# Kernel optimization log

Hardware: AMD Instinct MI355X
Metric: run time of the kernel (lower is better)

Reference implementation:

```python
import jax, jax.numpy as jnp
import numpy as np

B, CIN, COUT, K, SDIM, H, W = 8, 512, 256, 3, 512, 64, 64


def _blur_kernel():
    k = jnp.array([1.0, 3.0, 3.0, 1.0], dtype=jnp.float32)
    k = k[None, :] * k[:, None]
    k = k / k.sum()
    return k * 4.0  # upsample_factor ** 2


def setup_inputs() -> dict:
    key = jax.random.key(0)
    ks = jax.random.split(key, 4)
    return {
        "x": jax.random.normal(ks[0], (B, CIN, H, W), jnp.float32),
        "style": jax.random.normal(ks[1], (B, SDIM), jnp.float32),
        "weight": jax.random.normal(ks[2], (1, COUT, CIN, K, K), jnp.float32),
        "mod_weight": jax.random.normal(ks[3], (CIN, SDIM), jnp.float32),
        "mod_bias": jnp.ones((CIN,), jnp.float32),
    }


def reference(x, style, weight, mod_weight, mod_bias):
    b, cin, h, w = x.shape
    cout = weight.shape[1]
    k = weight.shape[-1]
    scale = 1.0 / np.sqrt(cin * k * k)          # fan_in of conv weight
    mod_scale = 1.0 / np.sqrt(mod_weight.shape[1])  # EqualLinear scale

    # modulation: EqualLinear(style) -> [B, Cin]
    s = style @ (mod_weight * mod_scale).T + mod_bias

    # per-sample modulated + demodulated weight [B, Cout, Cin, K, K]
    wmod = scale * weight * s[:, None, :, None, None]
    demod = jax.lax.rsqrt(jnp.sum(wmod * wmod, axis=(2, 3, 4)) + 1e-8)
    wmod = wmod * demod[:, :, None, None, None]

    # conv_transpose2d(stride=2, padding=0) == dilated conv with lhs_dilation=2,
    # padding K-1 on each side, spatially flipped kernel. Output (H-1)*2 + K.
    wflip = jnp.flip(wmod, axis=(-2, -1))

    def per_sample(xi, wi):
        return jax.lax.conv_general_dilated(
            xi[None], wi, window_strides=(1, 1),
            padding=[(k - 1, k - 1)] * 2, lhs_dilation=(2, 2),
            dimension_numbers=("NCHW", "OIHW", "NCHW"))[0]

    out = jax.vmap(per_sample)(x, wflip)  # [B, Cout, 2H+1, 2W+1] for K=3

    # Blur (upfirdn2d, up=1): torch does conv2d with flip(kernel);
    # lax conv is also correlation, so use flipped kernel, depthwise.
    bk = jnp.flip(_blur_kernel(), (0, 1))
    p = 4 - 2 - (k - 1)
    pad0 = (p + 1) // 2 + 1
    pad1 = p // 2 + 1
    wblur = jnp.broadcast_to(bk[None, None], (cout, 1, 4, 4))
    out = jax.lax.conv_general_dilated(
        out, wblur, (1, 1), [(pad0, pad1), (pad0, pad1)],
        feature_group_count=cout,
        dimension_numbers=("NCHW", "OIHW", "NCHW"))
    return out  # [B, Cout, 2H, 2W]
```

## Files before the change

### kernel.cpp

```cpp
#include <hip/hip_runtime.h>
#include <hip/hip_bf16.h>
#include <stdint.h>

typedef unsigned short u16;
typedef __attribute__((ext_vector_type(8))) short short8;
typedef __attribute__((ext_vector_type(4))) float floatx4;

__device__ __forceinline__ u16 f2bf(float f) {
    union { unsigned int i; float f; } v; v.f = f;
    unsigned int r = v.i + 0x7fff + ((v.i >> 16) & 1);
    return (u16)(r >> 16);
}

#define OFF_S    0
#define OFF_DEM  16384
#define OFF_W2   32768
#define OFF_BM   1048576
#define OFF_XMT  16777216

__global__ void k_style(const float* __restrict__ style, const float* __restrict__ mw,
                        const float* __restrict__ mb, float* __restrict__ S) {
    int g = blockIdx.x * 4 + (threadIdx.x >> 6);
    int lane = threadIdx.x & 63;
    int b = g >> 9, ci = g & 511;
    const float* sr = style + b * 512 + lane * 8;
    const float* wr = mw + ci * 512 + lane * 8;
    float4 s0 = *(const float4*)(sr);
    float4 s1 = *(const float4*)(sr + 4);
    float4 w0 = *(const float4*)(wr);
    float4 w1 = *(const float4*)(wr + 4);
    float acc = s0.x * w0.x + s0.y * w0.y + s0.z * w0.z + s0.w * w0.w
              + s1.x * w1.x + s1.y * w1.y + s1.z * w1.z + s1.w * w1.w;
    #pragma unroll
    for (int o = 32; o; o >>= 1) acc += __shfl_xor(acc, o, 64);
    if (lane == 0) S[g] = acc * 0.044194173824159216f + mb[ci];
}

__global__ void k_w2(const float* __restrict__ w, float* __restrict__ W2) {
    int t = blockIdx.x * 256 + threadIdx.x;
    const float* p = w + t * 9;
    float a = 0.f;
    #pragma unroll
    for (int i = 0; i < 9; ++i) { float v = p[i]; a += v * v; }
    W2[t] = a;
}

__global__ void k_demod(const float* __restrict__ W2, const float* __restrict__ S,
                        float* __restrict__ D) {
    int g = blockIdx.x * 4 + (threadIdx.x >> 6);
    int lane = threadIdx.x & 63;
    int b = g >> 8, co = g & 255;
    const float* wr = W2 + co * 512 + lane * 8;
    const float* sr = S + b * 512 + lane * 8;
    float4 w0 = *(const float4*)(wr);
    float4 w1 = *(const float4*)(wr + 4);
    float4 s0 = *(const float4*)(sr);
    float4 s1 = *(const float4*)(sr + 4);
    float a = w0.x * s0.x * s0.x + w0.y * s0.y * s0.y + w0.z * s0.z * s0.z + w0.w * s0.w * s0.w
            + w1.x * s1.x * s1.x + w1.y * s1.y * s1.y + w1.z * s1.z * s1.z + w1.w * s1.w * s1.w;
    #pragma unroll
    for (int o = 32; o; o >>= 1) a += __shfl_xor(a, o, 64);
    if (lane == 0) D[g] = 0.014731391274719738f * rsqrtf(a * (1.0f / 4608.0f) + 1e-8f);
}

__global__ void k_bmat(const float* __restrict__ Wt, u16* __restrict__ Bm) {
    __shared__ float wl[2304];
    int blk = blockIdx.x;
    int tid = threadIdx.x;
    int ci0 = (blk & 1) * 256;
    int co  = (blk >> 1) & 255;
    int p   = blk >> 9;
    int py = p >> 1, px = p & 1;
    int wbase = co * 4608 + ci0 * 9;
    #pragma unroll
    for (int j = 0; j < 9; ++j) wl[j * 256 + tid] = Wt[wbase + j * 256 + tid];
    __syncthreads();
    const float KT[2][3][3] = {
        {{0.f,1.f,3.f},{3.f,3.f,1.f},{1.f,0.f,0.f}},
        {{0.f,0.f,1.f},{1.f,3.f,3.f},{3.f,1.f,0.f}}
    };
    float wv[3][3];
    #pragma unroll
    for (int a = 0; a < 3; ++a)
        #pragma unroll
        for (int bq = 0; bq < 3; ++bq) wv[a][bq] = wl[tid * 9 + a * 3 + bq];
    int ci = ci0 + tid;
    int n = py * 512 + co * 2 + px;
    size_t base = (size_t)n * 4608 + ci;
    #pragma unroll
    for (int dyi = 0; dyi < 3; ++dyi) {
        #pragma unroll
        for (int dxi = 0; dxi < 3; ++dxi) {
            float val = 0.f;
            #pragma unroll
            for (int a = 0; a < 3; ++a) {
                float ky = KT[py][dyi][a];
                #pragma unroll
                for (int bq = 0; bq < 3; ++bq)
                    val += wv[a][bq] * (ky * KT[px][dxi][bq]);
            }
            Bm[base + (dyi * 3 + dxi) * 512] = f2bf(val * 0.0625f);
        }
    }
}

__global__ void k_fill(const float* __restrict__ X, const float* __restrict__ S,
                       u16* __restrict__ XMT) {
    __shared__ __align__(16) u16 tile[64][80];
    int blk = blockIdx.x;
    int ci0g = (blk & 7) * 64;
    int h = (blk >> 3) & 63;
    int b = blk >> 9;
    int t = threadIdx.x;
    if (t < 16) {
        int x = (t >> 3) ? 65 : 0;
        int c8 = t & 7;
        *(short8*)(XMT + ((size_t)(b * 66 + h + 1) * 66 + x) * 512 + ci0g + c8 * 8) = (short8)0;
    }
    if (h == 0 || h == 63) {
        int y = (h == 0) ? 0 : 65;
        for (int s0 = t; s0 < 528; s0 += 256) {
            int x = s0 >> 3, c8 = s0 & 7;
            *(short8*)(XMT + ((size_t)(b * 66 + y) * 66 + x) * 512 + ci0g + c8 * 8) = (short8)0;
        }
    }
    #pragma unroll
    for (int it = 0; it < 4; ++it) {
        int idx = it * 256 + t;
        int ci_l = idx >> 4, ch = idx & 15;
        float4 v = *(const float4*)(X + (((b * 512 + ci0g + ci_l) * 64 + h) * 64 + ch * 4));
        float s = S[b * 512 + ci0g + ci_l];
        int cisw = ci_l ^ ((ch & 7) << 3);
        tile[ch * 4 + 0][cisw] = f2bf(v.x * s);
        tile[ch * 4 + 1][cisw] = f2bf(v.y * s);
        tile[ch * 4 + 2][cisw] = f2bf(v.z * s);
        tile[ch * 4 + 3][cisw] = f2bf(v.w * s);
    }
    __syncthreads();
    #pragma unroll
    for (int it = 0; it < 2; ++it) {
        int idx = it * 256 + t;
        int wl = idx >> 3, c8 = idx & 7;
        short8 v = *(const short8*)(&tile[wl][(c8 ^ ((wl >> 2) & 7)) * 8]);
        *(short8*)(XMT + (((size_t)(b * 66 + h + 1) * 66 + (wl + 1)) * 512 + ci0g + c8 * 8)) = v;
    }
}


#define GLDS(SRC, DST) __builtin_amdgcn_global_load_lds( \
    (const __attribute__((address_space(1))) void*)(SRC), \
    (__attribute__((address_space(3))) void*)(DST), 16, 0, 0)

#define BAR() do { asm volatile("" ::: "memory"); \
                   __builtin_amdgcn_s_barrier(); \
                   asm volatile("" ::: "memory"); } while (0)

#define WAITV(n) asm volatile("s_waitcnt vmcnt(" #n ")" ::: "memory")

#define STAGE_A(d, h, kt) do { int _o = offA(kt); \
    GLDS(X  + preA[h][0] + _o, smem + (d)*32768 + (h)*16384 + t*16); \
    GLDS(X  + preA[h][1] + _o, smem + (d)*32768 + (h)*16384 + 8192 + t*16); \
  } while (0)
#define STAGE_B(d, h, kt) do { int _o = (kt)*64; \
    GLDS(Bm + preB[h][0] + _o, smem + 65536 + (d)*32768 + (h)*16384 + t*16); \
    GLDS(Bm + preB[h][1] + _o, smem + 65536 + (d)*32768 + (h)*16384 + 8192 + t*16); \
  } while (0)

#define LOAD_A(d, mh) do { \
    _Pragma("unroll") \
    for (int mt_ = 0; mt_ < 4; ++mt_) { \
      afr[mt_][0] = *(const short8*)(smem + (d)*32768 + (mh)*16384 + mt_*2048 + baseMA + cb0); \
      afr[mt_][1] = *(const short8*)(smem + (d)*32768 + (mh)*16384 + mt_*2048 + baseMA + cb1); \
    } } while (0)
#define LOAD_B(d, nh, DST) do { \
    _Pragma("unroll") \
    for (int nt_ = 0; nt_ < 2; ++nt_) { \
      DST[nt_][0] = *(const short8*)(smem + 65536 + (d)*32768 + (nh)*16384 + nt_*2048 + baseNB + cb0); \
      DST[nt_][1] = *(const short8*)(smem + 65536 + (d)*32768 + (nh)*16384 + nt_*2048 + baseNB + cb1); \
    } } while (0)

#define MMA(mh, nh, BF) do { \
    __builtin_amdgcn_s_setprio(1); \
    _Pragma("unroll") \
    for (int mt_ = 0; mt_ < 4; ++mt_) \
      _Pragma("unroll") \
      for (int nt_ = 0; nt_ < 2; ++nt_) { \
        acc[mh][mt_][nh][nt_] = __builtin_amdgcn_mfma_f32_16x16x32_bf16( \
            afr[mt_][0], BF[nt_][0], acc[mh][mt_][nh][nt_], 0, 0, 0); \
        acc[mh][mt_][nh][nt_] = __builtin_amdgcn_mfma_f32_16x16x32_bf16( \
            afr[mt_][1], BF[nt_][1], acc[mh][mt_][nh][nt_], 0, 0, 0); \
      } \
    __builtin_amdgcn_s_setprio(0); \
  } while (0)

__global__ __launch_bounds__(512, 2)
void k_main8(const u16* __restrict__ X, const u16* __restrict__ Bm,
             const float* __restrict__ D, float* __restrict__ out) {
    __shared__ __align__(16) char smem[131072];
    const int t = threadIdx.x;
    const int swz = (blockIdx.x & 7) * 64 + (blockIdx.x >> 3);
    const int bn = swz & 3, bm = swz >> 2;
    const int w = t >> 6, L = t & 63;
    const int wm = w >> 2, wn = w & 3;
    const int quad = L >> 4, col = L & 15;

    int preA[2][2], preB[2][2];
    #pragma unroll
    for (int h = 0; h < 2; ++h)
      #pragma unroll
      for (int i = 0; i < 2; ++i) {
        int sig = i * 512 + t;
        int ml = sig >> 3;
        int ks = (sig & 7) ^ (ml & 7);
        int mg = bm * 256 + h * 128 + ml;
        int b_ = mg >> 12, r = (mg >> 6) & 63, c = mg & 63;
        preA[h][i] = ((b_ * 66 + r) * 66 + c) * 512 + ks * 8;
        int ng = bn * 256 + h * 128 + ml;
        preB[h][i] = ng * 4608 + ks * 8;
      }
    auto offA = [](int kt) {
        int j = kt >> 3;
        int dy = (j * 11) >> 5;
        int dx = j - dy * 3;
        return (dy * 66 + dx) * 512 + (kt & 7) * 64;
    };

    const int baseMA = (wm * 64 + col) * 128;
    const int baseNB = (wn * 32 + col) * 128;
    const int cb0 = ((0 * 4 + quad) ^ (col & 7)) * 16;
    const int cb1 = ((1 * 4 + quad) ^ (col & 7)) * 16;

    short8 afr[4][2], bf0[2][2], bf1[2][2];
    floatx4 acc[2][4][2][2];
    #pragma unroll
    for (int mh = 0; mh < 2; ++mh)
      #pragma unroll
      for (int mt = 0; mt < 4; ++mt)
        #pragma unroll
        for (int nh = 0; nh < 2; ++nh)
          #pragma unroll
          for (int nt = 0; nt < 2; ++nt)
            acc[mh][mt][nh][nt] = (floatx4){0.f, 0.f, 0.f, 0.f};

    STAGE_A(0, 0, 0); STAGE_B(0, 0, 0);
    STAGE_A(0, 1, 0); STAGE_B(0, 1, 0);
    STAGE_A(1, 0, 1); STAGE_B(1, 0, 1);
    WAITV(4);
    BAR();

    #pragma unroll 1
    for (int it = 0; it < 35; ++it) {
        const int k = 2 * it;
        LOAD_A(0, 0); LOAD_B(0, 0, bf0);
        STAGE_A(1, 1, k + 1);
        BAR(); MMA(0, 0, bf0); BAR();
        LOAD_B(0, 1, bf1);
        STAGE_B(1, 1, k + 1);
        BAR(); MMA(0, 1, bf1); BAR();
        LOAD_A(0, 1);
        STAGE_A(0, 0, k + 2);
        BAR(); MMA(1, 0, bf0); BAR();
        STAGE_B(0, 0, k + 2);
        WAITV(4);
        BAR(); MMA(1, 1, bf1); BAR();
        LOAD_A(1, 0); LOAD_B(1, 0, bf0);
        STAGE_A(0, 1, k + 2);
        BAR(); MMA(0, 0, bf0); BAR();
        LOAD_B(1, 1, bf1);
        STAGE_B(0, 1, k + 2);
        BAR(); MMA(0, 1, bf1); BAR();
        LOAD_A(1, 1);
        STAGE_A(1, 0, k + 3);
        BAR(); MMA(1, 0, bf0); BAR();
        STAGE_B(1, 0, k + 3);
        WAITV(4);
        BAR(); MMA(1, 1, bf1); BAR();
    }

    LOAD_A(0, 0); LOAD_B(0, 0, bf0);
    STAGE_A(1, 1, 71);
    BAR(); MMA(0, 0, bf0); BAR();
    LOAD_B(0, 1, bf1);
    STAGE_B(1, 1, 71);
    BAR(); MMA(0, 1, bf1); BAR();
    LOAD_A(0, 1);
    BAR(); MMA(1, 0, bf0); BAR();
    WAITV(0);
    BAR(); MMA(1, 1, bf1); BAR();
    LOAD_A(1, 0); LOAD_B(1, 0, bf0);
    BAR(); MMA(0, 0, bf0); BAR();
    LOAD_B(1, 1, bf1);
    BAR(); MMA(0, 1, bf1); BAR();
    LOAD_A(1, 1);
    BAR(); MMA(1, 0, bf0); BAR();
    BAR(); MMA(1, 1, bf1); BAR();

    const int b   = bm >> 4;
    const int r0  = (bm & 15) * 4;
    const int py  = bn >> 1;
    const int co0 = (bn & 1) * 128;
    float dvals[2][2];
    #pragma unroll
    for (int nh = 0; nh < 2; ++nh)
      #pragma unroll
      for (int nt = 0; nt < 2; ++nt)
        dvals[nh][nt] = D[b * 256 + co0 + nh * 64 + wn * 16 + nt * 8 + (col >> 1)];

    float* ep = (float*)smem;
    #pragma unroll
    for (int rl = 0; rl < 4; ++rl) {
        if (wm == (rl & 1)) {
            const int mh = rl >> 1;
            #pragma unroll
            for (int nh = 0; nh < 2; ++nh)
              #pragma unroll
              for (int nt = 0; nt < 2; ++nt) {
                float dsv = dvals[nh][nt];
                int coL = nh * 64 + wn * 16 + nt * 8 + (col >> 1);
                #pragma unroll
                for (int mt = 0; mt < 4; ++mt)
                  #pragma unroll
                  for (int reg = 0; reg < 4; ++reg) {
                    int x = 2 * (mt * 16 + quad * 4 + reg) + (col & 1);
                    ep[coL * 132 + x] = acc[mh][mt][nh][nt][reg] * dsv;
                  }
              }
        }
        __syncthreads();
        #pragma unroll
        for (int itc = 0; itc < 8; ++itc) {
            int s = itc * 512 + t;
            int co = s >> 5, xi = s & 31;
            float4 v = *(const float4*)(ep + co * 132 + xi * 4);
            size_t o = ((size_t)((b * 256 + co0 + co) * 128 + (2 * (r0 + rl) + py))) * 128 + xi * 4;
            *(float4*)(out + o) = v;
        }
        __syncthreads();
    }
}

extern "C" void kernel_launch(void* const* d_in, const int* in_sizes, int n_in,
                              void* d_out, int out_size, void* d_ws, size_t ws_size,
                              hipStream_t stream) {
    const float* x      = (const float*)d_in[0];
    const float* style  = (const float*)d_in[1];
    const float* weight = (const float*)d_in[2];
    const float* mw     = (const float*)d_in[3];
    const float* mb     = (const float*)d_in[4];
    float* out = (float*)d_out;
    char* ws = (char*)d_ws;
    float* S   = (float*)(ws + OFF_S);
    float* DEM = (float*)(ws + OFF_DEM);
    float* W2  = (float*)(ws + OFF_W2);
    u16*  BM   = (u16*)(ws + OFF_BM);
    u16*  XMT  = (u16*)(ws + OFF_XMT);

    k_style<<<1024, 256, 0, stream>>>(style, mw, mb, S);
    k_w2   <<<512,  256, 0, stream>>>(weight, W2);
    k_demod<<<512,  256, 0, stream>>>(W2, S, DEM);
    k_bmat <<<2048, 256, 0, stream>>>(weight, BM);
    k_fill <<<4096, 256, 0, stream>>>(x, S, XMT);
    k_main8<<<512,  512, 0, stream>>>(XMT, BM, DEM, out);
}
```

Measured before the change: 428.4 us.

## Fuse preprocessing kernels into one launch and compute demod in main epilogue

Merges the style, weight-norm, B-matrix and input-fill kernels into a single heterogeneous k_pre launch. Each fill block now recomputes its 64 style scales locally and handles two rows. Demodulation is moved into the GEMM epilogue, which reads W2 and S directly and reduces per block. This cuts six launches to two and removes serial dependencies between tiny kernels, at the cost of redundant style dot products across blocks and extra epilogue work in the main kernel.

After: 455.8 us. 1.06x slower.

```diff
diff --git a/kernel.cpp b/kernel.cpp
--- a/kernel.cpp
+++ b/kernel.cpp
@@ -13,136 +13,125 @@
 }
 
 #define OFF_S    0
-#define OFF_DEM  16384
 #define OFF_W2   32768
 #define OFF_BM   1048576
 #define OFF_XMT  16777216
 
-__global__ void k_style(const float* __restrict__ style, const float* __restrict__ mw,
-                        const float* __restrict__ mb, float* __restrict__ S) {
-    int g = blockIdx.x * 4 + (threadIdx.x >> 6);
-    int lane = threadIdx.x & 63;
-    int b = g >> 9, ci = g & 511;
-    const float* sr = style + b * 512 + lane * 8;
-    const float* wr = mw + ci * 512 + lane * 8;
-    float4 s0 = *(const float4*)(sr);
-    float4 s1 = *(const float4*)(sr + 4);
-    float4 w0 = *(const float4*)(wr);
-    float4 w1 = *(const float4*)(wr + 4);
-    float acc = s0.x * w0.x + s0.y * w0.y + s0.z * w0.z + s0.w * w0.w
-              + s1.x * w1.x + s1.y * w1.y + s1.z * w1.z + s1.w * w1.w;
-    #pragma unroll
-    for (int o = 32; o; o >>= 1) acc += __shfl_xor(acc, o, 64);
-    if (lane == 0) S[g] = acc * 0.044194173824159216f + mb[ci];
-}
-
-__global__ void k_w2(const float* __restrict__ w, float* __restrict__ W2) {
-    int t = blockIdx.x * 256 + threadIdx.x;
-    const float* p = w + t * 9;
-    float a = 0.f;
-    #pragma unroll
-    for (int i = 0; i < 9; ++i) { float v = p[i]; a += v * v; }
-    W2[t] = a;
-}
-
-__global__ void k_demod(const float* __restrict__ W2, const float* __restrict__ S,
-                        float* __restrict__ D) {
-    int g = blockIdx.x * 4 + (threadIdx.x >> 6);
-    int lane = threadIdx.x & 63;
-    int b = g >> 8, co = g & 255;
-    const float* wr = W2 + co * 512 + lane * 8;
-    const float* sr = S + b * 512 + lane * 8;
-    float4 w0 = *(const float4*)(wr);
-    float4 w1 = *(const float4*)(wr + 4);
-    float4 s0 = *(const float4*)(sr);
-    float4 s1 = *(const float4*)(sr + 4);
-    float a = w0.x * s0.x * s0.x + w0.y * s0.y * s0.y + w0.z * s0.z * s0.z + w0.w * s0.w * s0.w
-            + w1.x * s1.x * s1.x + w1.y * s1.y * s1.y + w1.z * s1.z * s1.z + w1.w * s1.w * s1.w;
-    #pragma unroll
-    for (int o = 32; o; o >>= 1) a += __shfl_xor(a, o, 64);
-    if (lane == 0) D[g] = 0.014731391274719738f * rsqrtf(a * (1.0f / 4608.0f) + 1e-8f);
-}
-
-__global__ void k_bmat(const float* __restrict__ Wt, u16* __restrict__ Bm) {
-    __shared__ float wl[2304];
-    int blk = blockIdx.x;
-    int tid = threadIdx.x;
-    int ci0 = (blk & 1) * 256;
-    int co  = (blk >> 1) & 255;
-    int p   = blk >> 9;
-    int py = p >> 1, px = p & 1;
-    int wbase = co * 4608 + ci0 * 9;
-    #pragma unroll
-    for (int j = 0; j < 9; ++j) wl[j * 256 + tid] = Wt[wbase + j * 256 + tid];
-    __syncthreads();
-    const float KT[2][3][3] = {
-        {{0.f,1.f,3.f},{3.f,3.f,1.f},{1.f,0.f,0.f}},
-        {{0.f,0.f,1.f},{1.f,3.f,3.f},{3.f,1.f,0.f}}
-    };
-    float wv[3][3];
-    #pragma unroll
-    for (int a = 0; a < 3; ++a)
-        #pragma unroll
-        for (int bq = 0; bq < 3; ++bq) wv[a][bq] = wl[tid * 9 + a * 3 + bq];
-    int ci = ci0 + tid;
-    int n = py * 512 + co * 2 + px;
-    size_t base = (size_t)n * 4608 + ci;
-    #pragma unroll
-    for (int dyi = 0; dyi < 3; ++dyi) {
-        #pragma unroll
-        for (int dxi = 0; dxi < 3; ++dxi) {
-            float val = 0.f;
-            #pragma unroll
-            for (int a = 0; a < 3; ++a) {
-                float ky = KT[py][dyi][a];
+__global__ void k_pre(const float* __restrict__ X, const float* __restrict__ style,
+                      const float* __restrict__ mw, const float* __restrict__ mb,
+                      const float* __restrict__ Wt, float* __restrict__ W2,
+                      float* __restrict__ S, u16* __restrict__ Bm,
+                      u16* __restrict__ XMT) {
+    __shared__ __align__(16) char sm[20736];
+    const int bid = blockIdx.x;
+    const int t = threadIdx.x;
+
+    if (bid < 2048) {
+        u16 (*tile)[64][80] = (u16 (*)[64][80])sm;
+        float* sbuf = (float*)(sm + 20480);
+        const int g = bid & 7, hp = (bid >> 3) & 31, b = bid >> 8;
+        const int h0 = hp * 2;
+        const int lane = t & 63, wv = t >> 6;
+        {
+            const float* st = style + b * 512 + lane * 8;
+            float4 s0 = *(const float4*)st;
+            float4 s1 = *(const float4*)(st + 4);
+            for (int j = 0; j < 16; ++j) {
+                int cl = wv * 16 + j;
+                const float* wr = mw + (g * 64 + cl) * 512 + lane * 8;
+                float4 w0 = *(const float4*)wr;
+                float4 w1 = *(const float4*)(wr + 4);
+                float a = s0.x * w0.x + s0.y * w0.y + s0.z * w0.z + s0.w * w0.w
+                        + s1.x * w1.x + s1.y * w1.y + s1.z * w1.z + s1.w * w1.w;
                 #pragma unroll
-                for (int bq = 0; bq < 3; ++bq)
-                    val += wv[a][bq] * (ky * KT[px][dxi][bq]);
+                for (int o = 32; o; o >>= 1) a += __shfl_xor(a, o, 64);
+                if (lane == 0) sbuf[cl] = a * 0.044194173824159216f + mb[g * 64 + cl];
             }
-            Bm[base + (dyi * 3 + dxi) * 512] = f2bf(val * 0.0625f);
-        }
-    }
-}
-
-__global__ void k_fill(const float* __restrict__ X, const float* __restrict__ S,
-                       u16* __restrict__ XMT) {
-    __shared__ __align__(16) u16 tile[64][80];
-    int blk = blockIdx.x;
-    int ci0g = (blk & 7) * 64;
-    int h = (blk >> 3) & 63;
-    int b = blk >> 9;
-    int t = threadIdx.x;
-    if (t < 16) {
-        int x = (t >> 3) ? 65 : 0;
-        int c8 = t & 7;
-        *(short8*)(XMT + ((size_t)(b * 66 + h + 1) * 66 + x) * 512 + ci0g + c8 * 8) = (short8)0;
-    }
-    if (h == 0 || h == 63) {
-        int y = (h == 0) ? 0 : 65;
-        for (int s0 = t; s0 < 528; s0 += 256) {
-            int x = s0 >> 3, c8 = s0 & 7;
-            *(short8*)(XMT + ((size_t)(b * 66 + y) * 66 + x) * 512 + ci0g + c8 * 8) = (short8)0;
-        }
-    }
-    #pragma unroll
-    for (int it = 0; it < 4; ++it) {
-        int idx = it * 256 + t;
-        int ci_l = idx >> 4, ch = idx & 15;
-        float4 v = *(const float4*)(X + (((b * 512 + ci0g + ci_l) * 64 + h) * 64 + ch * 4));
-        float s = S[b * 512 + ci0g + ci_l];
-        int cisw = ci_l ^ ((ch & 7) << 3);
-        tile[ch * 4 + 0][cisw] = f2bf(v.x * s);
-        tile[ch * 4 + 1][cisw] = f2bf(v.y * s);
-        tile[ch * 4 + 2][cisw] = f2bf(v.z * s);
-        tile[ch * 4 + 3][cisw] = f2bf(v.w * s);
-    }
-    __syncthreads();
-    #pragma unroll
-    for (int it = 0; it < 2; ++it) {
-        int idx = it * 256 + t;
-        int wl = idx >> 3, c8 = idx & 7;
-        short8 v = *(const short8*)(&tile[wl][(c8 ^ ((wl >> 2) & 7)) * 8]);
-        *(short8*)(XMT + (((size_t)(b * 66 + h + 1) * 66 + (wl + 1)) * 512 + ci0g + c8 * 8)) = v;
+        }
+        __syncthreads();
+        if (hp == 0 && t < 64) S[b * 512 + g * 64 + t] = sbuf[t];
+        #pragma unroll
+        for (int hh = 0; hh < 2; ++hh) {
+            int h = h0 + hh;
+            if (t < 16) {
+                int x = (t >> 3) ? 65 : 0;
+                int c8 = t & 7;
+                *(short8*)(XMT + ((size_t)(b * 66 + h + 1) * 66 + x) * 512 + g * 64 + c8 * 8) = (short8)0;
+            }
+            if (h == 0 || h == 63) {
+                int y = (h == 0) ? 0 : 65;
+                for (int s0i = t; s0i < 528; s0i += 256) {
+                    int x = s0i >> 3, c8 = s0i & 7;
+                    *(short8*)(XMT + ((size_t)(b * 66 + y) * 66 + x) * 512 + g * 64 + c8 * 8) = (short8)0;
+                }
+            }
+        }
+        #pragma unroll
+        for (int it = 0; it < 8; ++it) {
+            int idx = it * 256 + t;
+            int hh = idx >> 10, idx2 = idx & 1023;
+            int ci_l = idx2 >> 4, ch = idx2 & 15;
+            float4 v = *(const float4*)(X + (((b * 512 + g * 64 + ci_l) * 64 + h0 + hh) * 64 + ch * 4));
+            float s = sbuf[ci_l];
+            int cisw = ci_l ^ ((ch & 7) << 3);
+            tile[hh][ch * 4 + 0][cisw] = f2bf(v.x * s);
+            tile[hh][ch * 4 + 1][cisw] = f2bf(v.y * s);
+            tile[hh][ch * 4 + 2][cisw] = f2bf(v.z * s);
+            tile[hh][ch * 4 + 3][cisw] = f2bf(v.w * s);
+        }
+        __syncthreads();
+        #pragma unroll
+        for (int it = 0; it < 4; ++it) {
+            int idx = it * 256 + t;
+            int hh = idx >> 9, idx2 = idx & 511;
+            int wl_ = idx2 >> 3, c8 = idx2 & 7;
+            short8 v = *(const short8*)(&tile[hh][wl_][(c8 ^ ((wl_ >> 2) & 7)) * 8]);
+            *(short8*)(XMT + (((size_t)(b * 66 + h0 + hh + 1) * 66 + (wl_ + 1)) * 512 + g * 64 + c8 * 8)) = v;
+        }
+    } else {
+        float* wl2 = (float*)sm;
+        const int bq = bid - 2048;
+        const int ci0 = (bq & 1) * 256;
+        const int co  = (bq >> 1) & 255;
+        const int p   = bq >> 9;
+        const int py = p >> 1, px = p & 1;
+        int wbase = co * 4608 + ci0 * 9;
+        #pragma unroll
+        for (int j = 0; j < 9; ++j) wl2[j * 256 + t] = Wt[wbase + j * 256 + t];
+        __syncthreads();
+        if (p == 0) {
+            float a = 0.f;
+            #pragma unroll
+            for (int j = 0; j < 9; ++j) { float v = wl2[t * 9 + j]; a += v * v; }
+            W2[co * 512 + ci0 + t] = a;
+        }
+        const float KT[2][3][3] = {
+            {{0.f,1.f,3.f},{3.f,3.f,1.f},{1.f,0.f,0.f}},
+            {{0.f,0.f,1.f},{1.f,3.f,3.f},{3.f,1.f,0.f}}
+        };
+        float wv[3][3];
+        #pragma unroll
+        for (int a = 0; a < 3; ++a)
+            #pragma unroll
+            for (int bq2 = 0; bq2 < 3; ++bq2) wv[a][bq2] = wl2[t * 9 + a * 3 + bq2];
+        int ci = ci0 + t;
+        int n = py * 512 + co * 2 + px;
+        size_t base = (size_t)n * 4608 + ci;
+        #pragma unroll
+        for (int dyi = 0; dyi < 3; ++dyi) {
+            #pragma unroll
+            for (int dxi = 0; dxi < 3; ++dxi) {
+                float val = 0.f;
+                #pragma unroll
+                for (int a = 0; a < 3; ++a) {
+                    float ky = KT[py][dyi][a];
+                    #pragma unroll
+                    for (int bq2 = 0; bq2 < 3; ++bq2)
+                        val += wv[a][bq2] * (ky * KT[px][dxi][bq2]);
+                }
+                Bm[base + (dyi * 3 + dxi) * 512] = f2bf(val * 0.0625f);
+            }
+        }
     }
 }
 
@@ -195,7 +184,8 @@
 
 __global__ __launch_bounds__(512, 2)
 void k_main8(const u16* __restrict__ X, const u16* __restrict__ Bm,
-             const float* __restrict__ D, float* __restrict__ out) {
+             const float* __restrict__ W2, const float* __restrict__ S,
+             float* __restrict__ out) {
     __shared__ __align__(16) char smem[131072];
     const int t = threadIdx.x;
     const int swz = (blockIdx.x & 7) * 64 + (blockIdx.x >> 3);
@@ -299,12 +289,32 @@
     const int r0  = (bm & 15) * 4;
     const int py  = bn >> 1;
     const int co0 = (bn & 1) * 128;
+    float* dls = (float*)(smem + 130560);
+    {
+        const float* srow = S + b * 512 + L * 8;
+        float4 sa = *(const float4*)srow;
+        float4 sb = *(const float4*)(srow + 4);
+        float s2_0 = sa.x * sa.x, s2_1 = sa.y * sa.y, s2_2 = sa.z * sa.z, s2_3 = sa.w * sa.w;
+        float s2_4 = sb.x * sb.x, s2_5 = sb.y * sb.y, s2_6 = sb.z * sb.z, s2_7 = sb.w * sb.w;
+        for (int j = 0; j < 16; ++j) {
+            int co_r = w * 16 + j;
+            const float* wr = W2 + (co0 + co_r) * 512 + L * 8;
+            float4 wa = *(const float4*)wr;
+            float4 wb = *(const float4*)(wr + 4);
+            float a = wa.x * s2_0 + wa.y * s2_1 + wa.z * s2_2 + wa.w * s2_3
+                    + wb.x * s2_4 + wb.y * s2_5 + wb.z * s2_6 + wb.w * s2_7;
+            #pragma unroll
+            for (int o = 32; o; o >>= 1) a += __shfl_xor(a, o, 64);
+            if (L == 0) dls[co_r] = 0.014731391274719738f * rsqrtf(a * (1.0f / 4608.0f) + 1e-8f);
+        }
+    }
+    __syncthreads();
     float dvals[2][2];
     #pragma unroll
     for (int nh = 0; nh < 2; ++nh)
       #pragma unroll
       for (int nt = 0; nt < 2; ++nt)
-        dvals[nh][nt] = D[b * 256 + co0 + nh * 64 + wn * 16 + nt * 8 + (col >> 1)];
+        dvals[nh][nt] = dls[nh * 64 + wn * 16 + nt * 8 + (col >> 1)];
 
     float* ep = (float*)smem;
     #pragma unroll
@@ -350,15 +360,10 @@
     float* out = (float*)d_out;
     char* ws = (char*)d_ws;
     float* S   = (float*)(ws + OFF_S);
-    float* DEM = (float*)(ws + OFF_DEM);
     float* W2  = (float*)(ws + OFF_W2);
     u16*  BM   = (u16*)(ws + OFF_BM);
     u16*  XMT  = (u16*)(ws + OFF_XMT);
 
-    k_style<<<1024, 256, 0, stream>>>(style, mw, mb, S);
-    k_w2   <<<512,  256, 0, stream>>>(weight, W2);
-    k_demod<<<512,  256, 0, stream>>>(W2, S, DEM);
-    k_bmat <<<2048, 256, 0, stream>>>(weight, BM);
-    k_fill <<<4096, 256, 0, stream>>>(x, S, XMT);
-    k_main8<<<512,  512, 0, stream>>>(XMT, BM, DEM, out);
+    k_pre  <<<4096, 256, 0, stream>>>(x, style, mw, mb, weight, W2, S, BM, XMT);
+    k_main8<<<512,  512, 0, stream>>>(XMT, BM, W2, S, out);
 }
```
